# Optimization experiments

Hardware: AMD Instinct MI355X
Metric: run time of the kernel (lower is better)

Reference implementation:

```python
import jax, jax.numpy as jnp
import numpy as np

VOCAB, EMBED, HIDDEN, NUM_CLASSES, PAD_IDX = 50257, 128, 128, 4, 0
B, T = 256, 512


def setup_inputs() -> dict:
    key = jax.random.key(0)
    ks = jax.random.split(key, 10)
    x = jax.random.randint(ks[0], (B, T), 0, VOCAB)
    h0 = jnp.zeros((B, HIDDEN), dtype=jnp.float32)
    # embedding: uniform(-0.1, 0.1), pad row zeroed (matches init_weights)
    emb = jax.random.uniform(ks[1], (VOCAB, EMBED), jnp.float32, -0.1, 0.1)
    emb = emb.at[PAD_IDX].set(0.0)
    def xavier(k, shape):
        fan_out, fan_in = shape
        bound = float(np.sqrt(6.0 / (fan_in + fan_out)))
        return jax.random.uniform(k, shape, jnp.float32, -bound, bound)
    W_ih = xavier(ks[2], (HIDDEN, EMBED))      # rnn.weight_ih_l0
    W_hh = xavier(ks[3], (HIDDEN, HIDDEN))     # rnn.weight_hh_l0
    b_ih = jnp.zeros((HIDDEN,), jnp.float32)
    b_hh = jnp.zeros((HIDDEN,), jnp.float32)
    W1 = xavier(ks[4], (2 * HIDDEN, HIDDEN))   # output_layer1
    b1 = jnp.zeros((2 * HIDDEN,), jnp.float32)
    W2 = xavier(ks[5], (NUM_CLASSES, 2 * HIDDEN))  # output_layer2
    b2 = jnp.zeros((NUM_CLASSES,), jnp.float32)
    return {"x": x, "h0": h0, "emb": emb, "W_ih": W_ih, "W_hh": W_hh,
            "b_ih": b_ih, "b_hh": b_hh, "W1": W1, "b1": b1, "W2": W2, "b2": b2}


def reference(x, h0, emb, W_ih, W_hh, b_ih, b_hh, W1, b1, W2, b2):
    # Embedding lookup (dropout layers are identity in eval mode)
    embedded = emb[x]                                    # [B, T, E]
    # Precompute input projection for every step, then scan the recurrence.
    x_proj = jnp.einsum('bte,he->bth', embedded, W_ih) + b_ih + b_hh  # [B, T, H]
    x_proj_t = jnp.swapaxes(x_proj, 0, 1)                # [T, B, H]

    def step(h, xp):
        h_new = jnp.tanh(xp + h @ W_hh.T)                # [B, H]
        return h_new, None

    last_hidden, _ = jax.lax.scan(step, h0, x_proj_t)    # [B, H]
    # MLP head: Linear -> ReLU -> Linear
    hidden_mlp = jax.nn.relu(last_hidden @ W1.T + b1)    # [B, 2H]
    logits = hidden_mlp @ W2.T + b2                      # [B, C]
    return (logits, last_hidden)
```

## Files before the change

### kernel.cpp

```cpp
#include <hip/hip_runtime.h>
#include <hip/hip_bf16.h>
#include <math.h>

#define BB 256
#define TT 512
#define EE 128
#define HH 128
#define NC 4
#define MM (BB * TT)

typedef __bf16 bf16x8 __attribute__((ext_vector_type(8)));
typedef __bf16 bf16x4 __attribute__((ext_vector_type(4)));
typedef float  f32x4  __attribute__((ext_vector_type(4)));
typedef float  f32x2  __attribute__((ext_vector_type(2)));

__device__ __forceinline__ float fast_tanh(float x) {
    float t = __builtin_amdgcn_exp2f(x * 2.885390081777927f);
    return 1.f - 2.f * __builtin_amdgcn_rcpf(1.f + t);
}

__device__ __forceinline__ void lds_barrier() {
    asm volatile("s_waitcnt lgkmcnt(0)" ::: "memory");
    __builtin_amdgcn_s_barrier();
    asm volatile("" ::: "memory");
}

template <typename XPT>
__global__ __launch_bounds__(256, 2) void embed_gemm(
    const int* __restrict__ x, const float* __restrict__ emb,
    const float* __restrict__ Wih, const float* __restrict__ bih,
    const float* __restrict__ bhh, XPT* __restrict__ xpout)
{
    const int tid = threadIdx.x;
    const int m0  = blockIdx.x * 128;

    const int LDA = 72;
    __shared__ __bf16 Ah[128 * 72];
    __shared__ __bf16 Al[128 * 72];
    __shared__ __bf16 Wh[128 * 72];
    __shared__ __bf16 Wl[128 * 72];
    __shared__ float  bias_s[128];
    __shared__ int    gix[128];

    if (tid < 128) {
        gix[tid]    = x[m0 + tid];
        bias_s[tid] = bih[tid] + bhh[tid];
    }

    const int lane = tid & 63, wid = tid >> 6;
    const int col  = lane & 15, quad = lane >> 4;

    f32x4 acc[2][8];
#pragma unroll
    for (int mt = 0; mt < 2; ++mt)
#pragma unroll
        for (int nt = 0; nt < 8; ++nt) acc[mt][nt] = f32x4{0.f, 0.f, 0.f, 0.f};

    __syncthreads();

#pragma unroll
    for (int half = 0; half < 2; ++half) {
#pragma unroll
        for (int it = 0; it < 8; ++it) {
            int c   = it * 256 + tid;
            int row = c >> 4;
            int seg = c & 15;

            float4 wv = ((const float4*)Wih)[row * 32 + half * 16 + seg];
            bf16x4 wh, wl;
            wh[0] = (__bf16)wv.x; wl[0] = (__bf16)(wv.x - (float)wh[0]);
            wh[1] = (__bf16)wv.y; wl[1] = (__bf16)(wv.y - (float)wh[1]);
            wh[2] = (__bf16)wv.z; wl[2] = (__bf16)(wv.z - (float)wh[2]);
            wh[3] = (__bf16)wv.w; wl[3] = (__bf16)(wv.w - (float)wh[3]);
            *(bf16x4*)&Wh[row * LDA + seg * 4] = wh;
            *(bf16x4*)&Wl[row * LDA + seg * 4] = wl;

            int gi = gix[row];
            float4 av = ((const float4*)emb)[(size_t)gi * 32 + half * 16 + seg];
            bf16x4 ah, al;
            ah[0] = (__bf16)av.x; al[0] = (__bf16)(av.x - (float)ah[0]);
            ah[1] = (__bf16)av.y; al[1] = (__bf16)(av.y - (float)ah[1]);
            ah[2] = (__bf16)av.z; al[2] = (__bf16)(av.z - (float)ah[2]);
            ah[3] = (__bf16)av.w; al[3] = (__bf16)(av.w - (float)ah[3]);
            *(bf16x4*)&Ah[row * LDA + seg * 4] = ah;
            *(bf16x4*)&Al[row * LDA + seg * 4] = al;
        }
        __syncthreads();

#pragma unroll
        for (int kk = 0; kk < 2; ++kk) {
            bf16x8 afh[2], afl[2];
#pragma unroll
            for (int mt = 0; mt < 2; ++mt) {
                int ro = (wid * 32 + mt * 16 + col) * LDA + kk * 32 + quad * 8;
                afh[mt] = *(const bf16x8*)&Ah[ro];
                afl[mt] = *(const bf16x8*)&Al[ro];
            }
#pragma unroll
            for (int nt = 0; nt < 8; ++nt) {
                int ro = (nt * 16 + col) * LDA + kk * 32 + quad * 8;
                bf16x8 wfh = *(const bf16x8*)&Wh[ro];
                bf16x8 wfl = *(const bf16x8*)&Wl[ro];
#pragma unroll
                for (int mt = 0; mt < 2; ++mt) {
                    acc[mt][nt] = __builtin_amdgcn_mfma_f32_16x16x32_bf16(afh[mt], wfh, acc[mt][nt], 0, 0, 0);
                    acc[mt][nt] = __builtin_amdgcn_mfma_f32_16x16x32_bf16(afl[mt], wfh, acc[mt][nt], 0, 0, 0);
                    acc[mt][nt] = __builtin_amdgcn_mfma_f32_16x16x32_bf16(afh[mt], wfl, acc[mt][nt], 0, 0, 0);
                }
            }
        }
        if (half == 0) __syncthreads();
    }

#pragma unroll
    for (int mt = 0; mt < 2; ++mt) {
#pragma unroll
        for (int nt = 0; nt < 8; ++nt) {
            int m = m0 + wid * 32 + mt * 16 + quad * 4;
            int n = nt * 16 + col;
            float bs = bias_s[n];
#pragma unroll
            for (int r = 0; r < 4; ++r)
                xpout[(size_t)(m + r) * 128 + n] = (XPT)(acc[mt][nt][r] + bs);
        }
    }
}

template <typename XPT>
__global__ __launch_bounds__(256, 1) void rnn_scan(
    const XPT* __restrict__ xp, const float* __restrict__ Whh,
    const float* __restrict__ h0, float* __restrict__ hlast)
{
    const int b    = blockIdx.x;
    const int tid  = threadIdx.x;
    const int w    = tid >> 6;
    const int lane = tid & 63;
    const int o    = lane & 31;
    const int kh   = lane >> 5;

    __shared__ float h_s[2][128];

    f32x4 wv[16];
    {
        const float* r = Whh + (size_t)(w * 32 + o) * 128 + kh * 64;
#pragma unroll
        for (int c = 0; c < 16; ++c) wv[c] = *(const f32x4*)(r + c * 4);
    }
#pragma unroll
    for (int c = 0; c < 16; ++c) asm volatile("" : "+v"(wv[c]));

    if (tid < 128) h_s[0][tid] = h0[b * 128 + tid];

    const XPT* xpb  = xp + (size_t)b * (TT * 128);
    const int  xoff = w * 32 + o;
    float xv[8];
#pragma unroll
    for (int s = 0; s < 8; ++s) xv[s] = (float)xpb[s * 128 + xoff];
    lds_barrier();

    for (int tw = 0; tw < TT; tw += 8) {
#pragma unroll
        for (int ts = 0; ts < 8; ++ts) {
            const int c = ts & 1;
            const float* hq = &h_s[c][kh * 64];
            f32x4 h4[16];
#pragma unroll
            for (int u = 0; u < 16; ++u) h4[u] = *(const f32x4*)&hq[u * 4];

            f32x4 aA = f32x4{0.f, 0.f, 0.f, 0.f};
            f32x4 aB = f32x4{0.f, 0.f, 0.f, 0.f};
#pragma unroll
            for (int u = 0; u < 8; ++u) {
                aA += wv[u]     * h4[u];
                aB += wv[u + 8] * h4[u + 8];
            }
            f32x4 at = aA + aB;
            float p  = (at[0] + at[1]) + (at[2] + at[3]);
            p += __shfl_xor(p, 32, 64);
            float hnew = fast_tanh(p + xv[ts]);

            if (lane < 32) h_s[c ^ 1][w * 32 + o] = hnew;
            if (tw + 8 < TT)
                xv[ts] = (float)xpb[(size_t)(tw + 8 + ts) * 128 + xoff];
            lds_barrier();
        }
    }
    if (tid < 128) hlast[b * 128 + tid] = h_s[0][tid];
}

__global__ __launch_bounds__(256, 2) void mlp_head(
    const float* __restrict__ hlast, const float* __restrict__ W1,
    const float* __restrict__ b1, const float* __restrict__ W2,
    const float* __restrict__ b2, float* __restrict__ out)
{
    const int b = blockIdx.x, tid = threadIdx.x;
    __shared__ float h_row[128];
    __shared__ float hid[256];

    if (tid < 128) {
        float hv = hlast[b * 128 + tid];
        h_row[tid] = hv;
        out[1024 + b * 128 + tid] = hv;
    }
    __syncthreads();

    {
        float acc = b1[tid];
        const float4* wrow = (const float4*)(W1 + (size_t)tid * 128);
#pragma unroll
        for (int k4 = 0; k4 < 32; ++k4) {
            float4 wv = wrow[k4];
            acc += wv.x * h_row[k4 * 4 + 0] + wv.y * h_row[k4 * 4 + 1]
                 + wv.z * h_row[k4 * 4 + 2] + wv.w * h_row[k4 * 4 + 3];
        }
        hid[tid] = fmaxf(acc, 0.f);
    }
    __syncthreads();

    const int wv = tid >> 6, lane = tid & 63;
    float s = 0.f;
#pragma unroll
    for (int qq = 0; qq < 4; ++qq)
        s += hid[qq * 64 + lane] * W2[wv * 256 + qq * 64 + lane];
#pragma unroll
    for (int off = 32; off > 0; off >>= 1) s += __shfl_down(s, off);
    if (lane == 0) out[b * 4 + wv] = s + b2[wv];
}

extern "C" void kernel_launch(void* const* d_in, const int* in_sizes, int n_in,
                              void* d_out, int out_size, void* d_ws, size_t ws_size,
                              hipStream_t stream)
{
    const int*   x   = (const int*)d_in[0];
    const float* h0  = (const float*)d_in[1];
    const float* emb = (const float*)d_in[2];
    const float* Wih = (const float*)d_in[3];
    const float* Whh = (const float*)d_in[4];
    const float* bih = (const float*)d_in[5];
    const float* bhh = (const float*)d_in[6];
    const float* W1  = (const float*)d_in[7];
    const float* b1  = (const float*)d_in[8];
    const float* W2  = (const float*)d_in[9];
    const float* b2  = (const float*)d_in[10];
    float* out = (float*)d_out;

    const size_t xp_f32_bytes = (size_t)MM * 128 * sizeof(float);
    const size_t hl_bytes     = (size_t)BB * 128 * sizeof(float);

    if (ws_size >= xp_f32_bytes + hl_bytes) {
        float* xpw = (float*)d_ws;
        float* hl  = (float*)((char*)d_ws + xp_f32_bytes);
        embed_gemm<float><<<MM / 128, 256, 0, stream>>>(x, emb, Wih, bih, bhh, xpw);
        rnn_scan<float><<<BB, 256, 0, stream>>>(xpw, Whh, h0, hl);
        mlp_head<<<BB, 256, 0, stream>>>(hl, W1, b1, W2, b2, out);
    } else {
        __bf16* xpw = (__bf16*)d_ws;
        float*  hl  = (float*)((char*)d_ws + (size_t)MM * 128 * sizeof(__bf16));
        embed_gemm<__bf16><<<MM / 128, 256, 0, stream>>>(x, emb, Wih, bih, bhh, xpw);
        rnn_scan<__bf16><<<BB, 256, 0, stream>>>(xpw, Whh, h0, hl);
        mlp_head<<<BB, 256, 0, stream>>>(hl, W1, b1, W2, b2, out);
    }
}
```

Measured before the change: 283.4 us.

## Process four batch rows per block in RNN scan kernel

```diff
diff --git a/kernel.cpp b/kernel.cpp
--- a/kernel.cpp
+++ b/kernel.cpp
@@ -126,19 +126,20 @@
     }
 }
 
+#define BPB 4
 template <typename XPT>
 __global__ __launch_bounds__(256, 1) void rnn_scan(
     const XPT* __restrict__ xp, const float* __restrict__ Whh,
     const float* __restrict__ h0, float* __restrict__ hlast)
 {
-    const int b    = blockIdx.x;
+    const int b0   = blockIdx.x * BPB;
     const int tid  = threadIdx.x;
     const int w    = tid >> 6;
     const int lane = tid & 63;
     const int o    = lane & 31;
     const int kh   = lane >> 5;
 
-    __shared__ float h_s[2][128];
+    __shared__ float h_s[BPB][2][128];
 
     f32x4 wv[16];
     {
@@ -149,43 +150,56 @@
 #pragma unroll
     for (int c = 0; c < 16; ++c) asm volatile("" : "+v"(wv[c]));
 
-    if (tid < 128) h_s[0][tid] = h0[b * 128 + tid];
-
-    const XPT* xpb  = xp + (size_t)b * (TT * 128);
-    const int  xoff = w * 32 + o;
-    float xv[8];
-#pragma unroll
-    for (int s = 0; s < 8; ++s) xv[s] = (float)xpb[s * 128 + xoff];
+    if (tid < 128) {
+#pragma unroll
+        for (int bt = 0; bt < BPB; ++bt)
+            h_s[bt][0][tid] = h0[(b0 + bt) * 128 + tid];
+    }
+
+    const int xoff = w * 32 + o;
+    float xv[BPB][8];
+#pragma unroll
+    for (int bt = 0; bt < BPB; ++bt)
+#pragma unroll
+        for (int s = 0; s < 8; ++s)
+            xv[bt][s] = (float)xp[((size_t)(b0 + bt) * TT + s) * 128 + xoff];
     lds_barrier();
 
     for (int tw = 0; tw < TT; tw += 8) {
 #pragma unroll
         for (int ts = 0; ts < 8; ++ts) {
             const int c = ts & 1;
-            const float* hq = &h_s[c][kh * 64];
-            f32x4 h4[16];
-#pragma unroll
-            for (int u = 0; u < 16; ++u) h4[u] = *(const f32x4*)&hq[u * 4];
-
-            f32x4 aA = f32x4{0.f, 0.f, 0.f, 0.f};
-            f32x4 aB = f32x4{0.f, 0.f, 0.f, 0.f};
-#pragma unroll
-            for (int u = 0; u < 8; ++u) {
-                aA += wv[u]     * h4[u];
-                aB += wv[u + 8] * h4[u + 8];
+#pragma unroll
+            for (int bt = 0; bt < BPB; ++bt) {
+                const float* hq = &h_s[bt][c][kh * 64];
+                f32x4 h4[16];
+#pragma unroll
+                for (int u = 0; u < 16; ++u) h4[u] = *(const f32x4*)&hq[u * 4];
+
+                f32x4 aA = f32x4{0.f, 0.f, 0.f, 0.f};
+                f32x4 aB = f32x4{0.f, 0.f, 0.f, 0.f};
+#pragma unroll
+                for (int u = 0; u < 8; ++u) {
+                    aA += wv[u]     * h4[u];
+                    aB += wv[u + 8] * h4[u + 8];
+                }
+                f32x4 at = aA + aB;
+                float p  = (at[0] + at[1]) + (at[2] + at[3]);
+                p += __shfl_xor(p, 32, 64);
+                float hnew = fast_tanh(p + xv[bt][ts]);
+
+                if (lane < 32) h_s[bt][c ^ 1][w * 32 + o] = hnew;
+                if (tw + 8 < TT)
+                    xv[bt][ts] = (float)xp[((size_t)(b0 + bt) * TT + tw + 8 + ts) * 128 + xoff];
             }
-            f32x4 at = aA + aB;
-            float p  = (at[0] + at[1]) + (at[2] + at[3]);
-            p += __shfl_xor(p, 32, 64);
-            float hnew = fast_tanh(p + xv[ts]);
-
-            if (lane < 32) h_s[c ^ 1][w * 32 + o] = hnew;
-            if (tw + 8 < TT)
-                xv[ts] = (float)xpb[(size_t)(tw + 8 + ts) * 128 + xoff];
             lds_barrier();
         }
     }
-    if (tid < 128) hlast[b * 128 + tid] = h_s[0][tid];
+    if (tid < 128) {
+#pragma unroll
+        for (int bt = 0; bt < BPB; ++bt)
+            hlast[(b0 + bt) * 128 + tid] = h_s[bt][0][tid];
+    }
 }
 
 __global__ __launch_bounds__(256, 2) void mlp_head(
@@ -251,13 +265,13 @@
         float* xpw = (float*)d_ws;
         float* hl  = (float*)((char*)d_ws + xp_f32_bytes);
         embed_gemm<float><<<MM / 128, 256, 0, stream>>>(x, emb, Wih, bih, bhh, xpw);
-        rnn_scan<float><<<BB, 256, 0, stream>>>(xpw, Whh, h0, hl);
+        rnn_scan<float><<<BB / BPB, 256, 0, stream>>>(xpw, Whh, h0, hl);
         mlp_head<<<BB, 256, 0, stream>>>(hl, W1, b1, W2, b2, out);
     } else {
         __bf16* xpw = (__bf16*)d_ws;
         float*  hl  = (float*)((char*)d_ws + (size_t)MM * 128 * sizeof(__bf16));
         embed_gemm<__bf16><<<MM / 128, 256, 0, stream>>>(x, emb, Wih, bih, bhh, xpw);
-        rnn_scan<__bf16><<<BB, 256, 0, stream>>>(xpw, Whh, h0, hl);
+        rnn_scan<__bf16><<<BB / BPB, 256, 0, stream>>>(xpw, Whh, h0, hl);
         mlp_head<<<BB, 256, 0, stream>>>(hl, W1, b1, W2, b2, out);
     }
 }
```

Result: slower. 749.5 us (+164.5%).

## Batch RNN scan across 16 sequences per block using split-bf16 MFMA

Applied to the files above, without the earlier changes.

```diff
diff --git a/kernel.cpp b/kernel.cpp
--- a/kernel.cpp
+++ b/kernel.cpp
@@ -127,65 +127,130 @@
 }
 
 template <typename XPT>
-__global__ __launch_bounds__(256, 1) void rnn_scan(
+__device__ __forceinline__ f32x4 load_xp4(const XPT* p) {
+    if constexpr (sizeof(XPT) == 4) {
+        return *(const f32x4*)p;
+    } else {
+        bf16x4 v = *(const bf16x4*)p;
+        return f32x4{(float)v[0], (float)v[1], (float)v[2], (float)v[3]};
+    }
+}
+
+#define SB 16
+template <typename XPT>
+__global__ __launch_bounds__(128, 1) void rnn_scan(
     const XPT* __restrict__ xp, const float* __restrict__ Whh,
     const float* __restrict__ h0, float* __restrict__ hlast)
 {
-    const int b    = blockIdx.x;
     const int tid  = threadIdx.x;
     const int w    = tid >> 6;
-    const int lane = tid & 63;
-    const int o    = lane & 31;
-    const int kh   = lane >> 5;
-
-    __shared__ float h_s[2][128];
-
-    f32x4 wv[16];
-    {
-        const float* r = Whh + (size_t)(w * 32 + o) * 128 + kh * 64;
-#pragma unroll
-        for (int c = 0; c < 16; ++c) wv[c] = *(const f32x4*)(r + c * 4);
-    }
-#pragma unroll
-    for (int c = 0; c < 16; ++c) asm volatile("" : "+v"(wv[c]));
-
-    if (tid < 128) h_s[0][tid] = h0[b * 128 + tid];
-
-    const XPT* xpb  = xp + (size_t)b * (TT * 128);
-    const int  xoff = w * 32 + o;
-    float xv[8];
-#pragma unroll
-    for (int s = 0; s < 8; ++s) xv[s] = (float)xpb[s * 128 + xoff];
+    const int l    = tid & 63;
+    const int col  = l & 15;
+    const int quad = l >> 4;
+    const int bg   = blockIdx.x * SB;
+
+    __shared__ __bf16 Hh[2][SB * 128];
+    __shared__ __bf16 Hl[2][SB * 128];
+
+    bf16x8 Wf_h[4][4], Wf_l[4][4];
+#pragma unroll
+    for (int ht = 0; ht < 4; ++ht)
+#pragma unroll
+        for (int kt = 0; kt < 4; ++kt) {
+            const float* src = Whh + (size_t)(w * 64 + ht * 16 + col) * 128
+                             + kt * 32 + quad * 8;
+            float4 a = *(const float4*)(src);
+            float4 b = *(const float4*)(src + 4);
+            float v[8] = {a.x, a.y, a.z, a.w, b.x, b.y, b.z, b.w};
+            bf16x8 hi, lo;
+#pragma unroll
+            for (int j = 0; j < 8; ++j) {
+                hi[j] = (__bf16)v[j];
+                lo[j] = (__bf16)(v[j] - (float)hi[j]);
+            }
+            Wf_h[ht][kt] = hi; Wf_l[ht][kt] = lo;
+        }
+#pragma unroll
+    for (int ht = 0; ht < 4; ++ht)
+#pragma unroll
+        for (int kt = 0; kt < 4; ++kt)
+            asm volatile("" : "+v"(Wf_h[ht][kt]), "+v"(Wf_l[ht][kt]));
+
+#pragma unroll
+    for (int i = 0; i < SB * 128; i += 128) {
+        int idx = i + tid, b = idx >> 7, h = idx & 127;
+        float v = h0[(bg + b) * 128 + h];
+        __bf16 hi = (__bf16)v;
+        int e = b * 128 + (h ^ ((b & 7) << 3));
+        Hh[0][e] = hi;
+        Hl[0][e] = (__bf16)(v - (float)hi);
+    }
+
+    const XPT* xpb = xp + (size_t)(bg + col) * TT * 128 + w * 64 + quad * 4;
+    f32x4 xv[2][4];
+#pragma unroll
+    for (int s = 0; s < 2; ++s)
+#pragma unroll
+        for (int ht = 0; ht < 4; ++ht)
+            xv[s][ht] = load_xp4(xpb + (size_t)s * 128 + ht * 16);
+
     lds_barrier();
 
-    for (int tw = 0; tw < TT; tw += 8) {
-#pragma unroll
-        for (int ts = 0; ts < 8; ++ts) {
-            const int c = ts & 1;
-            const float* hq = &h_s[c][kh * 64];
-            f32x4 h4[16];
-#pragma unroll
-            for (int u = 0; u < 16; ++u) h4[u] = *(const f32x4*)&hq[u * 4];
-
-            f32x4 aA = f32x4{0.f, 0.f, 0.f, 0.f};
-            f32x4 aB = f32x4{0.f, 0.f, 0.f, 0.f};
-#pragma unroll
-            for (int u = 0; u < 8; ++u) {
-                aA += wv[u]     * h4[u];
-                aB += wv[u + 8] * h4[u + 8];
-            }
-            f32x4 at = aA + aB;
-            float p  = (at[0] + at[1]) + (at[2] + at[3]);
-            p += __shfl_xor(p, 32, 64);
-            float hnew = fast_tanh(p + xv[ts]);
-
-            if (lane < 32) h_s[c ^ 1][w * 32 + o] = hnew;
-            if (tw + 8 < TT)
-                xv[ts] = (float)xpb[(size_t)(tw + 8 + ts) * 128 + xoff];
-            lds_barrier();
-        }
-    }
-    if (tid < 128) hlast[b * 128 + tid] = h_s[0][tid];
+#define SCAN_STEP(t, par)                                                     \
+    {                                                                         \
+        bf16x8 Hf_h[4], Hf_l[4];                                              \
+        _Pragma("unroll")                                                     \
+        for (int kt = 0; kt < 4; ++kt) {                                      \
+            int e = col * 128 + ((kt * 32 + quad * 8) ^ ((col & 7) << 3));    \
+            Hf_h[kt] = *(const bf16x8*)&Hh[par][e];                           \
+            Hf_l[kt] = *(const bf16x8*)&Hl[par][e];                           \
+        }                                                                     \
+        size_t roff = (size_t)((t) + 2 < TT ? (t) + 2 : TT - 1) * 128;        \
+        f32x4 acc[4];                                                         \
+        _Pragma("unroll")                                                     \
+        for (int ht = 0; ht < 4; ++ht) acc[ht] = f32x4{0.f, 0.f, 0.f, 0.f};   \
+        _Pragma("unroll")                                                     \
+        for (int kt = 0; kt < 4; ++kt) {                                      \
+            _Pragma("unroll")                                                 \
+            for (int ht = 0; ht < 4; ++ht) {                                  \
+                acc[ht] = __builtin_amdgcn_mfma_f32_16x16x32_bf16(            \
+                    Wf_h[ht][kt], Hf_h[kt], acc[ht], 0, 0, 0);                \
+                acc[ht] = __builtin_amdgcn_mfma_f32_16x16x32_bf16(            \
+                    Wf_l[ht][kt], Hf_h[kt], acc[ht], 0, 0, 0);                \
+                acc[ht] = __builtin_amdgcn_mfma_f32_16x16x32_bf16(            \
+                    Wf_h[ht][kt], Hf_l[kt], acc[ht], 0, 0, 0);                \
+            }                                                                 \
+        }                                                                     \
+        _Pragma("unroll")                                                     \
+        for (int ht = 0; ht < 4; ++ht) {                                      \
+            bf16x4 hh, hl;                                                    \
+            _Pragma("unroll")                                                 \
+            for (int r = 0; r < 4; ++r) {                                     \
+                float hn = fast_tanh(acc[ht][r] + xv[par][ht][r]);            \
+                hh[r] = (__bf16)hn;                                           \
+                hl[r] = (__bf16)(hn - (float)hh[r]);                          \
+            }                                                                 \
+            xv[par][ht] = load_xp4(xpb + roff + ht * 16);                     \
+            int hb = w * 64 + ht * 16 + quad * 4;                             \
+            int e  = col * 128 + (hb ^ ((col & 7) << 3));                     \
+            *(bf16x4*)&Hh[(par) ^ 1][e] = hh;                                 \
+            *(bf16x4*)&Hl[(par) ^ 1][e] = hl;                                 \
+        }                                                                     \
+        lds_barrier();                                                        \
+    }
+
+    for (int t = 0; t < TT; t += 2) {
+        SCAN_STEP(t, 0)
+        SCAN_STEP(t + 1, 1)
+    }
+#undef SCAN_STEP
+
+#pragma unroll
+    for (int i = 0; i < SB * 128; i += 128) {
+        int idx = i + tid, b = idx >> 7, h = idx & 127;
+        int e = b * 128 + (h ^ ((b & 7) << 3));
+        hlast[(bg + b) * 128 + h] = (float)Hh[0][e] + (float)Hl[0][e];
+    }
 }
 
 __global__ __launch_bounds__(256, 2) void mlp_head(
@@ -251,13 +316,13 @@
         float* xpw = (float*)d_ws;
         float* hl  = (float*)((char*)d_ws + xp_f32_bytes);
         embed_gemm<float><<<MM / 128, 256, 0, stream>>>(x, emb, Wih, bih, bhh, xpw);
-        rnn_scan<float><<<BB, 256, 0, stream>>>(xpw, Whh, h0, hl);
+        rnn_scan<float><<<BB / SB, 128, 0, stream>>>(xpw, Whh, h0, hl);
         mlp_head<<<BB, 256, 0, stream>>>(hl, W1, b1, W2, b2, out);
     } else {
         __bf16* xpw = (__bf16*)d_ws;
         float*  hl  = (float*)((char*)d_ws + (size_t)MM * 128 * sizeof(__bf16));
         embed_gemm<__bf16><<<MM / 128, 256, 0, stream>>>(x, emb, Wih, bih, bhh, xpw);
-        rnn_scan<__bf16><<<BB, 256, 0, stream>>>(xpw, Whh, h0, hl);
+        rnn_scan<__bf16><<<BB / SB, 128, 0, stream>>>(xpw, Whh, h0, hl);
         mlp_head<<<BB, 256, 0, stream>>>(hl, W1, b1, W2, b2, out);
     }
 }
```

Result: slower. 533.7 us (+88.3%).

## Split RNN scan into quarter-K lanes computing two outputs each with swizzled LDS

Applied to the files above, without the earlier changes.

```diff
diff --git a/kernel.cpp b/kernel.cpp
--- a/kernel.cpp
+++ b/kernel.cpp
@@ -23,6 +23,17 @@
     asm volatile("s_waitcnt lgkmcnt(0)" ::: "memory");
     __builtin_amdgcn_s_barrier();
     asm volatile("" ::: "memory");
+}
+
+__device__ __forceinline__ float xor16_sum(float p) {
+    float t1 = p, t2 = p;
+    asm volatile("v_permlane16_swap_b32 %0, %1" : "+v"(t1), "+v"(t2));
+    return t1 + t2;
+}
+__device__ __forceinline__ float xor32_sum(float p) {
+    float t1 = p, t2 = p;
+    asm volatile("v_permlane32_swap_b32 %0, %1" : "+v"(t1), "+v"(t2));
+    return t1 + t2;
 }
 
 template <typename XPT>
@@ -135,57 +146,80 @@
     const int tid  = threadIdx.x;
     const int w    = tid >> 6;
     const int lane = tid & 63;
-    const int o    = lane & 31;
-    const int kh   = lane >> 5;
+    const int oo   = lane & 15;
+    const int kq   = lane >> 4;
+
+    const int A = w * 32 + oo;
+    const int Bo = A + 16;
 
     __shared__ float h_s[2][128];
 
-    f32x4 wv[16];
-    {
-        const float* r = Whh + (size_t)(w * 32 + o) * 128 + kh * 64;
-#pragma unroll
-        for (int c = 0; c < 16; ++c) wv[c] = *(const f32x4*)(r + c * 4);
-    }
-#pragma unroll
-    for (int c = 0; c < 16; ++c) asm volatile("" : "+v"(wv[c]));
-
-    if (tid < 128) h_s[0][tid] = h0[b * 128 + tid];
-
-    const XPT* xpb  = xp + (size_t)b * (TT * 128);
-    const int  xoff = w * 32 + o;
-    float xv[8];
-#pragma unroll
-    for (int s = 0; s < 8; ++s) xv[s] = (float)xpb[s * 128 + xoff];
+    f32x4 wA[8], wB[8];
+#pragma unroll
+    for (int uu = 0; uu < 8; ++uu) {
+        int ul = (uu + 8 - kq) & 7;
+        wA[uu] = *(const f32x4*)(Whh + (size_t)A  * 128 + kq * 32 + ul * 4);
+        wB[uu] = *(const f32x4*)(Whh + (size_t)Bo * 128 + kq * 32 + ul * 4);
+    }
+#pragma unroll
+    for (int c = 0; c < 8; ++c)
+        asm volatile("" : "+v"(wA[c]), "+v"(wB[c]));
+
+    if (tid < 128) {
+        int q = tid >> 5, u = (tid >> 2) & 7, e = tid & 3;
+        h_s[0][q * 32 + ((u + q) & 7) * 4 + e] = h0[b * 128 + tid];
+    }
+
+    const int wiA = w * 32 + (((oo >> 2) + w) & 7) * 4 + (oo & 3);
+    const int wiB = w * 32 + ((4 + (oo >> 2) + w) & 7) * 4 + (oo & 3);
+
+    const XPT* xpb = xp + (size_t)b * (TT * 128);
+    float xvA[8], xvB[8];
+#pragma unroll
+    for (int s = 0; s < 8; ++s) {
+        xvA[s] = (float)xpb[s * 128 + A];
+        xvB[s] = (float)xpb[s * 128 + Bo];
+    }
     lds_barrier();
 
     for (int tw = 0; tw < TT; tw += 8) {
 #pragma unroll
         for (int ts = 0; ts < 8; ++ts) {
             const int c = ts & 1;
-            const float* hq = &h_s[c][kh * 64];
-            f32x4 h4[16];
-#pragma unroll
-            for (int u = 0; u < 16; ++u) h4[u] = *(const f32x4*)&hq[u * 4];
-
-            f32x4 aA = f32x4{0.f, 0.f, 0.f, 0.f};
-            f32x4 aB = f32x4{0.f, 0.f, 0.f, 0.f};
-#pragma unroll
-            for (int u = 0; u < 8; ++u) {
-                aA += wv[u]     * h4[u];
-                aB += wv[u + 8] * h4[u + 8];
-            }
-            f32x4 at = aA + aB;
-            float p  = (at[0] + at[1]) + (at[2] + at[3]);
-            p += __shfl_xor(p, 32, 64);
-            float hnew = fast_tanh(p + xv[ts]);
-
-            if (lane < 32) h_s[c ^ 1][w * 32 + o] = hnew;
-            if (tw + 8 < TT)
-                xv[ts] = (float)xpb[(size_t)(tw + 8 + ts) * 128 + xoff];
+            const float* hq = &h_s[c][kq * 32];
+            f32x4 h4[8];
+#pragma unroll
+            for (int uu = 0; uu < 8; ++uu) h4[uu] = *(const f32x4*)&hq[uu * 4];
+
+            f32x4 sA = f32x4{0.f, 0.f, 0.f, 0.f};
+            f32x4 sB = f32x4{0.f, 0.f, 0.f, 0.f};
+#pragma unroll
+            for (int uu = 0; uu < 8; ++uu) {
+                sA += wA[uu] * h4[uu];
+                sB += wB[uu] * h4[uu];
+            }
+            float pA = (sA[0] + sA[1]) + (sA[2] + sA[3]);
+            float pB = (sB[0] + sB[1]) + (sB[2] + sB[3]);
+            pA = xor16_sum(pA);  pB = xor16_sum(pB);
+            pA = xor32_sum(pA);  pB = xor32_sum(pB);
+
+            float hA = fast_tanh(pA + xvA[ts]);
+            float hB = fast_tanh(pB + xvB[ts]);
+            if (kq == 0) {
+                h_s[c ^ 1][wiA] = hA;
+                h_s[c ^ 1][wiB] = hB;
+            }
+            if (tw + 8 < TT) {
+                xvA[ts] = (float)xpb[(size_t)(tw + 8 + ts) * 128 + A];
+                xvB[ts] = (float)xpb[(size_t)(tw + 8 + ts) * 128 + Bo];
+            }
             lds_barrier();
         }
     }
-    if (tid < 128) hlast[b * 128 + tid] = h_s[0][tid];
+    if (tid < 128) {
+        int q = tid >> 5, u = (tid >> 2) & 7, e = tid & 3;
+        hlast[b * 128 + tid] = h_s[0][q * 32 + ((u + q) & 7) * 4 + e];
+    }
 }
 
 __global__ __launch_bounds__(256, 2) void mlp_head(
```

After: 279.3 us. About the same (-1.5%).
